# Kernel optimization log

Measured on AMD Instinct MI355X. Metric: run time of the kernel, lower is better.

## Reference

```python
import jax, jax.numpy as jnp
import numpy as np

H = 768       # hidden_size
HEADS = 8     # num_heads
T = 3         # num_timesteps
B = 128       # molecules in batch
N_ATOM = 48   # atoms per molecule
E_INTRA = 96  # intra-molecule directed edges per molecule
NPG = N_ATOM + 1          # nodes per graph (incl. virtual)
EPG = E_INTRA + N_ATOM    # edges per graph (incl. atom->virtual)
N = B * NPG
E = B * EPG


def setup_inputs() -> dict:
    key = jax.random.key(0)
    ks = jax.random.split(key, 10)
    atom_feat = jax.random.normal(ks[0], (B, N_ATOM, H), dtype=jnp.float32)
    mol_feat = jax.random.normal(ks[1], (B, H), dtype=jnp.float32)
    # node features with virtual node (=mol_feat) appended per graph, as in add_virtual_nodes_and_edges
    h_nodes = jnp.concatenate([atom_feat, mol_feat[:, None, :]], axis=1).reshape(N, H)
    off = jnp.arange(B, dtype=jnp.int32) * NPG
    intra_src = jax.random.randint(ks[2], (B, E_INTRA), 0, N_ATOM, dtype=jnp.int32) + off[:, None]
    intra_dst = jax.random.randint(ks[3], (B, E_INTRA), 0, N_ATOM, dtype=jnp.int32) + off[:, None]
    virt_src = jnp.arange(N_ATOM, dtype=jnp.int32)[None, :] + off[:, None]
    virt_dst = jnp.broadcast_to((off + N_ATOM)[:, None], (B, N_ATOM))
    src = jnp.concatenate([intra_src, virt_src], axis=1).reshape(E)
    dst = jnp.concatenate([intra_dst, virt_dst], axis=1).reshape(E)
    virtual_nids = off + N_ATOM  # last node of each graph (cumsum(batch_num_nodes)-1)
    attn_eids = ((jnp.arange(B, dtype=jnp.int32) * EPG)[:, None]
                 + E_INTRA + jnp.arange(N_ATOM, dtype=jnp.int32)[None, :]).reshape(-1)
    s = 0.02
    W_src = jax.random.normal(ks[4], (T, H, HEADS * H), dtype=jnp.float32) * s
    W_dst = jax.random.normal(ks[5], (T, H, HEADS * H), dtype=jnp.float32) * s
    attn_a = jax.random.normal(ks[6], (T, HEADS, H), dtype=jnp.float32) * s
    W_ih = jax.random.normal(ks[7], (T, 3 * H, H), dtype=jnp.float32) * s
    W_hh = jax.random.normal(ks[8], (T, 3 * H, H), dtype=jnp.float32) * s
    b_src = jnp.zeros((T, HEADS * H), jnp.float32)
    b_dst = jnp.zeros((T, HEADS * H), jnp.float32)
    b_ih = jnp.zeros((T, 3 * H), jnp.float32)
    b_hh = jnp.zeros((T, 3 * H), jnp.float32)
    return {"h_nodes": h_nodes, "mol_feat": mol_feat, "W_src": W_src, "b_src": b_src,
            "W_dst": W_dst, "b_dst": b_dst, "attn_a": attn_a, "W_ih": W_ih, "W_hh": W_hh,
            "b_ih": b_ih, "b_hh": b_hh, "src": src, "dst": dst,
            "virtual_nids": virtual_nids, "attn_eids": attn_eids}


def _gru_cell(x, hprev, W_ih_t, W_hh_t, b_ih_t, b_hh_t):
    # torch.nn.GRUCell: gates ordered r, z, n
    gi = x @ W_ih_t.T + b_ih_t
    gh = hprev @ W_hh_t.T + b_hh_t
    ir, iz, inn = jnp.split(gi, 3, axis=-1)
    hr, hz, hn = jnp.split(gh, 3, axis=-1)
    r = jax.nn.sigmoid(ir + hr)
    z = jax.nn.sigmoid(iz + hz)
    n = jnp.tanh(inn + r * hn)
    return (1.0 - z) * n + z * hprev


def _forward(h_nodes, mol_feat, W_src, b_src, W_dst, b_dst, attn_a,
             W_ih, W_hh, b_ih, b_hh, src, dst, virtual_nids, attn_eids):
    h = h_nodes
    mol_emb = mol_feat
    attns = []
    for t in range(T):
        # GATv2Conv (DGL, eval mode so feat_drop/attn_drop are identity)
        fs = (h @ W_src[t] + b_src[t]).reshape(N, HEADS, H)
        fd = (h @ W_dst[t] + b_dst[t]).reshape(N, HEADS, H)
        e = jax.nn.leaky_relu(fs[src] + fd[dst], negative_slope=0.2)  # [E, heads, H]
        logits = jnp.einsum('ehd,hd->eh', e, attn_a[t])               # [E, heads]
        # edge softmax over incoming edges per destination node
        m = jax.ops.segment_max(logits, dst, num_segments=N)
        ex = jnp.exp(logits - m[dst])
        ssum = jax.ops.segment_sum(ex, dst, num_segments=N)
        a = ex / ssum[dst]                                            # [E, heads]
        rst = jax.ops.segment_sum(a[:, :, None] * fs[src], dst, num_segments=N)  # [N, heads, H]
        h = rst.mean(axis=1)                                          # mean over heads
        out_virtual = h[virtual_nids]                                 # [B, H]
        mol_emb = jax.nn.relu(_gru_cell(out_virtual, mol_emb, W_ih[t], W_hh[t], b_ih[t], b_hh[t]))
        attns.append(a.mean(axis=1)[attn_eids])                       # attention on virtual edges
    return mol_emb, jnp.stack(attns)


def reference(h_nodes, mol_feat, W_src, b_src, W_dst, b_dst, attn_a,
              W_ih, W_hh, b_ih, b_hh, src, dst, virtual_nids, attn_eids):
    return _forward(h_nodes, mol_feat, W_src, b_src, W_dst, b_dst, attn_a,
                    W_ih, W_hh, b_ih, b_hh, src, dst, virtual_nids, attn_eids)
```

## Files before the change

kernel.cpp:

```cpp
#include <hip/hip_runtime.h>
#include <hip/hip_bf16.h>

typedef __hip_bfloat16 bf16;
typedef float f32x4 __attribute__((ext_vector_type(4)));
typedef __bf16 bf16x8 __attribute__((ext_vector_type(8)));
typedef short s16x8 __attribute__((ext_vector_type(8)));
typedef short s16x2 __attribute__((ext_vector_type(2)));

#define HDIM 768
#define NHEAD 8
#define BMOL 128
#define NPG 49
#define EPG 144
#define NNODE (BMOL * NPG)
#define NEDGE (BMOL * EPG)
#define NH 6144
#define G3 2304

__device__ __forceinline__ float b2f(short s) {
    unsigned int u = ((unsigned int)(unsigned short)s) << 16;
    return __builtin_bit_cast(float, u);
}

__device__ __forceinline__ void async16(const bf16* g, bf16* l) {
    __builtin_amdgcn_global_load_lds(
        (const __attribute__((address_space(1))) void*)g,
        (__attribute__((address_space(3))) void*)l, 16, 0, 0);
}

__global__ __launch_bounds__(256) void gemm_bt(
    const bf16* __restrict__ A, const bf16* __restrict__ Bt0,
    const bf16* __restrict__ Bt1, const float* __restrict__ bias0,
    const float* __restrict__ bias1, bf16* __restrict__ C0,
    bf16* __restrict__ C1, int M, int N, int K) {
    __shared__ __align__(16) bf16 lA[2 * 128 * 32];
    __shared__ __align__(16) bf16 lB[2 * 128 * 32];
    const int tid = threadIdx.x;
    const int lane = tid & 63;
    const int wave = tid >> 6;
    const int l16 = lane & 15;
    const int quad = lane >> 4;
    const int m0 = blockIdx.y * 128;
    const int n0 = blockIdx.x * 128;
    const bf16* Bt = blockIdx.z ? Bt1 : Bt0;
    const float* bias = blockIdx.z ? bias1 : bias0;
    bf16* C = blockIdx.z ? C1 : C0;

    const int r64 = tid >> 2;
    const int kc = (tid & 3) * 8;

    const bf16* gA = A + (size_t)(m0 + r64) * K + kc;
    const bf16* gB = Bt + (size_t)(n0 + r64) * K + kc;
    bf16* lAp = lA + tid * 8;
    bf16* lBp = lB + tid * 8;
    const size_t rstep = (size_t)64 * K;

    const int wm0 = (wave >> 1) * 64;
    const int wn0 = (wave & 1) * 64;

    f32x4 acc[4][4];
#pragma unroll
    for (int i = 0; i < 4; ++i)
#pragma unroll
        for (int j = 0; j < 4; ++j) acc[i][j] = (f32x4){0.f, 0.f, 0.f, 0.f};

    for (int k0 = 0; k0 < K; k0 += 64) {
        __syncthreads();
        async16(gA + k0, lAp);
        async16(gA + k0 + rstep, lAp + 2048);
        async16(gA + k0 + 32, lAp + 4096);
        async16(gA + k0 + 32 + rstep, lAp + 6144);
        async16(gB + k0, lBp);
        async16(gB + k0 + rstep, lBp + 2048);
        async16(gB + k0 + 32, lBp + 4096);
        async16(gB + k0 + 32 + rstep, lBp + 6144);
        __syncthreads();
#pragma unroll
        for (int ks = 0; ks < 2; ++ks) {
            bf16x8 af[4], bfr[4];
#pragma unroll
            for (int i = 0; i < 4; ++i)
                af[i] = *(const bf16x8*)(lA + ks * 4096 +
                                         (wm0 + i * 16 + l16) * 32 + quad * 8);
#pragma unroll
            for (int j = 0; j < 4; ++j)
                bfr[j] = *(const bf16x8*)(lB + ks * 4096 +
                                          (wn0 + j * 16 + l16) * 32 + quad * 8);
#pragma unroll
            for (int i = 0; i < 4; ++i)
#pragma unroll
                for (int j = 0; j < 4; ++j)
                    acc[i][j] = __builtin_amdgcn_mfma_f32_16x16x32_bf16(
                        af[i], bfr[j], acc[i][j], 0, 0, 0);
        }
    }

#pragma unroll
    for (int i = 0; i < 4; ++i) {
#pragma unroll
        for (int j = 0; j < 4; ++j) {
            int row = m0 + wm0 + i * 16 + quad * 4;
            int col = n0 + wn0 + j * 16 + l16;
            float bc = bias[col];
#pragma unroll
            for (int r = 0; r < 4; ++r)
                C[(size_t)(row + r) * N + col] =
                    __float2bfloat16(acc[i][j][r] + bc);
        }
    }
}

__global__ __launch_bounds__(256) void gemm_small(
    const bf16* __restrict__ hws, const int* __restrict__ vnids,
    const bf16* __restrict__ A1, const bf16* __restrict__ B0,
    const bf16* __restrict__ B1, const float* __restrict__ bias0,
    const float* __restrict__ bias1, float* __restrict__ C0,
    float* __restrict__ C1) {
    __shared__ __align__(16) bf16 lA[32 * 32];
    __shared__ __align__(16) bf16 lB[256 * 32];
    const int tid = threadIdx.x;
    const int lane = tid & 63;
    const int wave = tid >> 6;
    const int l16 = lane & 15;
    const int quad = lane >> 4;
    const int K = HDIM;
    const int y0 = blockIdx.y * 32;
    const int x0 = blockIdx.x * 256;
    const bf16* Bt = blockIdx.z ? B1 : B0;
    const float* bias = blockIdx.z ? bias1 : bias0;
    float* C = blockIdx.z ? C1 : C0;

    const int ry = y0 + (tid >> 2);
    const bf16* gA;
    if (blockIdx.z)
        gA = A1 + (size_t)ry * K + (tid & 3) * 8;
    else
        gA = hws + (size_t)vnids[ry & 127] * K + (tid & 3) * 8;
    const bf16* gB = Bt + (size_t)(x0 + (tid >> 2)) * K + (tid & 3) * 8;
    bf16* lAp = lA + tid * 8;
    bf16* lBp = lB + tid * 8;
    const size_t rstep = (size_t)64 * K;

    f32x4 acc[2][4];
#pragma unroll
    for (int i = 0; i < 2; ++i)
#pragma unroll
        for (int j = 0; j < 4; ++j) acc[i][j] = (f32x4){0.f, 0.f, 0.f, 0.f};

    for (int k0 = 0; k0 < K; k0 += 32) {
        __syncthreads();
        if (tid < 128) async16(gA + k0, lAp);
        async16(gB + k0, lBp);
        async16(gB + k0 + rstep, lBp + 2048);
        async16(gB + k0 + 2 * rstep, lBp + 4096);
        async16(gB + k0 + 3 * rstep, lBp + 6144);
        __syncthreads();
        bf16x8 af[2], bfr[4];
#pragma unroll
        for (int i = 0; i < 2; ++i)
            af[i] = *(const bf16x8*)(lA + (i * 16 + l16) * 32 + quad * 8);
#pragma unroll
        for (int j = 0; j < 4; ++j)
            bfr[j] = *(const bf16x8*)(lB + (wave * 64 + j * 16 + l16) * 32 +
                                      quad * 8);
#pragma unroll
        for (int i = 0; i < 2; ++i)
#pragma unroll
            for (int j = 0; j < 4; ++j)
                acc[i][j] = __builtin_amdgcn_mfma_f32_16x16x32_bf16(
                    af[i], bfr[j], acc[i][j], 0, 0, 0);
    }

#pragma unroll
    for (int i = 0; i < 2; ++i) {
#pragma unroll
        for (int j = 0; j < 4; ++j) {
            int row = y0 + i * 16 + quad * 4;
            int col = x0 + wave * 64 + j * 16 + l16;
            float bc = bias[col];
#pragma unroll
            for (int r = 0; r < 4; ++r)
                C[(size_t)(row + r) * G3 + col] = acc[i][j][r] + bc;
        }
    }
}

__global__ __launch_bounds__(256) void transpose_w(
    const float* __restrict__ W, bf16* __restrict__ Wt, int K, int Nn) {
    __shared__ bf16 tile[64][65];
    const int z = blockIdx.z;
    const float* Wp = W + (size_t)z * K * Nn;
    bf16* Wtp = Wt + (size_t)z * K * Nn;
    const int n0 = blockIdx.x * 64;
    const int k0 = blockIdx.y * 64;
    const int tx = threadIdx.x & 63;
    const int ty = threadIdx.x >> 6;
#pragma unroll
    for (int i = 0; i < 64; i += 4)
        tile[ty + i][tx] = __float2bfloat16(Wp[(size_t)(k0 + ty + i) * Nn + n0 + tx]);
    __syncthreads();
#pragma unroll
    for (int i = 0; i < 64; i += 4)
        Wtp[(size_t)(n0 + ty + i) * K + k0 + tx] = tile[tx][ty + i];
}

__global__ void cvt_kernel(const float* __restrict__ x, bf16* __restrict__ y,
                           int n) {
    int i = blockIdx.x * 256 + threadIdx.x;
    if (i < n) y[i] = __float2bfloat16(x[i]);
}

__global__ __launch_bounds__(256) void logits_kernel(
    const bf16* __restrict__ fs, const bf16* __restrict__ fd,
    const float* __restrict__ attn_a_t, const int* __restrict__ src,
    const int* __restrict__ dst, float* __restrict__ logits) {
    __shared__ __align__(16) float s_a[NH];
    const int tid = threadIdx.x;
    for (int p = tid; p < NH; p += 256) s_a[p] = attn_a_t[p];
    __syncthreads();

    const int wave = tid >> 6;
    const int lane = tid & 63;
    const int e = blockIdx.x * 4 + wave;
    const int gs = src[e], gd = dst[e];
    const bf16* ps = fs + (size_t)gs * NH;
    const bf16* pd = fd + (size_t)gd * NH;
    const int h = lane >> 3;
    const int s = lane & 7;
    const int base = h * HDIM + s * 8;

    float acc = 0.f;
#pragma unroll
    for (int j = 0; j < 12; ++j) {
        const int off = base + j * 64;
        s16x8 a8 = *(const s16x8*)(ps + off);
        s16x8 d8 = *(const s16x8*)(pd + off);
        f32x4 av0 = *(const f32x4*)(s_a + off);
        f32x4 av1 = *(const f32x4*)(s_a + off + 4);
#pragma unroll
        for (int u = 0; u < 4; ++u) {
            float x = b2f(a8[u]) + b2f(d8[u]);
            x = (x > 0.f) ? x : 0.2f * x;
            acc += x * av0[u];
        }
#pragma unroll
        for (int u = 0; u < 4; ++u) {
            float x = b2f(a8[4 + u]) + b2f(d8[4 + u]);
            x = (x > 0.f) ? x : 0.2f * x;
            acc += x * av1[u];
        }
    }
    acc += __shfl_xor(acc, 1);
    acc += __shfl_xor(acc, 2);
    acc += __shfl_xor(acc, 4);
    if (s == 0) logits[(size_t)e * NHEAD + h] = acc;
}

__global__ __launch_bounds__(256) void softmax_kernel(
    const float* __restrict__ logits, const int* __restrict__ dst,
    float* __restrict__ w, float* __restrict__ outv) {
    __shared__ float s_logit[EPG * NHEAD];
    __shared__ float s_w[EPG * NHEAD];
    __shared__ int s_ld[EPG];
    __shared__ float s_m[NPG * NHEAD], s_inv[NPG * NHEAD];
    const int tid = threadIdx.x;
    const int b = blockIdx.x;
    for (int p = tid; p < EPG * NHEAD; p += 256)
        s_logit[p] = logits[(size_t)b * EPG * NHEAD + p];
    if (tid < EPG) s_ld[tid] = dst[b * EPG + tid] - b * NPG;
    __syncthreads();

    for (int p = tid; p < NPG * NHEAD; p += 256) {
        int n = p >> 3, h = p & 7;
        float m = -3.0e38f;
        for (int le = 0; le < EPG; ++le)
            if (s_ld[le] == n) m = fmaxf(m, s_logit[le * NHEAD + h]);
        float ss = 0.f;
        for (int le = 0; le < EPG; ++le)
            if (s_ld[le] == n) ss += __expf(s_logit[le * NHEAD + h] - m);
        s_m[p] = m;
        s_inv[p] = (ss > 0.f) ? 1.f / ss : 0.f;
    }
    __syncthreads();

    for (int p = tid; p < EPG * NHEAD; p += 256) {
        int le = p >> 3, h = p & 7;
        int ld = s_ld[le];
        float a =
            0.125f * __expf(s_logit[p] - s_m[ld * NHEAD + h]) * s_inv[ld * NHEAD + h];
        s_w[p] = a;
        w[(size_t)b * EPG * NHEAD + p] = a;
    }
    __syncthreads();
    if (tid < 48) {
        float s = 0.f;
#pragma unroll
        for (int h = 0; h < NHEAD; ++h) s += s_w[(96 + tid) * NHEAD + h];
        outv[b * 48 + tid] = s;
    }
}

__global__ __launch_bounds__(256) void aggregate_kernel(
    const bf16* __restrict__ fs, const float* __restrict__ w,
    const int* __restrict__ src, const int* __restrict__ dst,
    bf16* __restrict__ hout) {
    __shared__ float acc[NPG * 128];
    __shared__ float s_w[EPG * NHEAD];
    __shared__ int s_gs[EPG], s_ld[EPG];
    const int tid = threadIdx.x;
    const int c = blockIdx.x;
    const int b = blockIdx.y;
    const int grp = tid >> 6;
    const int l = tid & 63;
    if (tid < EPG) {
        int e = b * EPG + tid;
        s_gs[tid] = src[e];
        s_ld[tid] = dst[e] - b * NPG;
    }
    for (int p = tid; p < EPG * NHEAD; p += 256)
        s_w[p] = w[(size_t)b * EPG * NHEAD + p];
    for (int p = tid; p < NPG * 128; p += 256) acc[p] = 0.f;
    __syncthreads();

    const int dim = c * 128 + l * 2;
    for (int le4 = 0; le4 < EPG; le4 += 4) {
        const int le = le4 + grp;
        const bf16* p = fs + (size_t)s_gs[le] * NH + dim;
        float sum0 = 0.f, sum1 = 0.f;
#pragma unroll
        for (int h = 0; h < NHEAD; ++h) {
            s16x2 v = *(const s16x2*)(p + h * HDIM);
            float wv = s_w[le * NHEAD + h];
            sum0 += wv * b2f(v[0]);
            sum1 += wv * b2f(v[1]);
        }
        float* ap = &acc[s_ld[le] * 128 + l * 2];
        atomicAdd(ap, sum0);
        atomicAdd(ap + 1, sum1);
    }
    __syncthreads();
    for (int p = tid; p < NPG * 128; p += 256) {
        int n = p >> 7, d = p & 127;
        hout[((size_t)b * NPG + n) * HDIM + c * 128 + d] =
            __float2bfloat16(acc[p]);
    }
}

__global__ void init_memb_kernel(const float* __restrict__ mf,
                                 float* __restrict__ m32,
                                 bf16* __restrict__ m16) {
    int idx = blockIdx.x * 256 + threadIdx.x;
    float f = mf[idx];
    m32[idx] = f;
    m16[idx] = __float2bfloat16(f);
}

__global__ void gru_gate_kernel(const float* __restrict__ gi,
                                const float* __restrict__ gh,
                                float* __restrict__ m32, bf16* __restrict__ m16,
                                float* __restrict__ outp, int last) {
    int idx = blockIdx.x * 256 + threadIdx.x;
    int b = idx / HDIM, d = idx - b * HDIM;
    const float* gib = gi + (size_t)b * G3;
    const float* ghb = gh + (size_t)b * G3;
    float ir = gib[d], iz = gib[HDIM + d], in_ = gib[2 * HDIM + d];
    float hr = ghb[d], hz = ghb[HDIM + d], hn = ghb[2 * HDIM + d];
    float r = 1.f / (1.f + __expf(-(ir + hr)));
    float z = 1.f / (1.f + __expf(-(iz + hz)));
    float n = tanhf(in_ + r * hn);
    float hprev = m32[idx];
    float hnew = (1.f - z) * n + z * hprev;
    hnew = fmaxf(hnew, 0.f);
    m32[idx] = hnew;
    m16[idx] = __float2bfloat16(hnew);
    if (last) outp[idx] = hnew;
}

extern "C" void kernel_launch(void* const* d_in, const int* in_sizes, int n_in,
                              void* d_out, int out_size, void* d_ws,
                              size_t ws_size, hipStream_t stream) {
    const float* h_nodes = (const float*)d_in[0];
    const float* mol_feat = (const float*)d_in[1];
    const float* W_src = (const float*)d_in[2];
    const float* b_src = (const float*)d_in[3];
    const float* W_dst = (const float*)d_in[4];
    const float* b_dst = (const float*)d_in[5];
    const float* attn_a = (const float*)d_in[6];
    const float* W_ih = (const float*)d_in[7];
    const float* W_hh = (const float*)d_in[8];
    const float* b_ih = (const float*)d_in[9];
    const float* b_hh = (const float*)d_in[10];
    const int* src = (const int*)d_in[11];
    const int* dst = (const int*)d_in[12];
    const int* vnids = (const int*)d_in[13];
    float* out = (float*)d_out;

    char* p = (char*)d_ws;
    auto alloc = [&](size_t bytes) {
        char* r = p;
        p += (bytes + 255) & ~(size_t)255;
        return r;
    };
    bf16* wsrcT = (bf16*)alloc((size_t)3 * NH * HDIM * 2);
    bf16* wdstT = (bf16*)alloc((size_t)3 * NH * HDIM * 2);
    bf16* wihB = (bf16*)alloc((size_t)3 * G3 * HDIM * 2);
    bf16* whhB = (bf16*)alloc((size_t)3 * G3 * HDIM * 2);
    bf16* fs = (bf16*)alloc((size_t)NNODE * NH * 2);
    bf16* fd = (bf16*)alloc((size_t)NNODE * NH * 2);
    bf16* h_ws = (bf16*)alloc((size_t)NNODE * HDIM * 2);
    float* lg = (float*)alloc((size_t)NEDGE * NHEAD * 4);
    float* w_e = (float*)alloc((size_t)NEDGE * NHEAD * 4);
    float* memb32 = (float*)alloc((size_t)BMOL * HDIM * 4);
    bf16* memb16 = (bf16*)alloc((size_t)BMOL * HDIM * 2);
    float* gi = (float*)alloc((size_t)BMOL * G3 * 4);
    float* gh = (float*)alloc((size_t)BMOL * G3 * 4);

    dim3 tgrid(NH / 64, HDIM / 64, 3);
    transpose_w<<<tgrid, 256, 0, stream>>>(W_src, wsrcT, HDIM, NH);
    transpose_w<<<tgrid, 256, 0, stream>>>(W_dst, wdstT, HDIM, NH);
    {
        int n = 3 * G3 * HDIM;
        cvt_kernel<<<(n + 255) / 256, 256, 0, stream>>>(W_ih, wihB, n);
        cvt_kernel<<<(n + 255) / 256, 256, 0, stream>>>(W_hh, whhB, n);
    }
    {
        int n = NNODE * HDIM;
        cvt_kernel<<<(n + 255) / 256, 256, 0, stream>>>(h_nodes, h_ws, n);
    }
    init_memb_kernel<<<BMOL * HDIM / 256, 256, 0, stream>>>(mol_feat, memb32,
                                                            memb16);

    for (int t = 0; t < 3; ++t) {
        gemm_bt<<<dim3(NH / 128, NNODE / 128, 2), 256, 0, stream>>>(
            h_ws, wsrcT + (size_t)t * NH * HDIM, wdstT + (size_t)t * NH * HDIM,
            b_src + (size_t)t * NH, b_dst + (size_t)t * NH, fs, fd, NNODE, NH,
            HDIM);
        logits_kernel<<<NEDGE / 4, 256, 0, stream>>>(
            fs, fd, attn_a + (size_t)t * NHEAD * HDIM, src, dst, lg);
        softmax_kernel<<<BMOL, 256, 0, stream>>>(
            lg, dst, w_e, out + BMOL * HDIM + t * BMOL * 48);
        aggregate_kernel<<<dim3(6, BMOL), 256, 0, stream>>>(fs, w_e, src, dst,
                                                            h_ws);
        gemm_small<<<dim3(G3 / 256, 4, 2), 256, 0, stream>>>(
            h_ws, vnids, memb16, wihB + (size_t)t * G3 * HDIM,
            whhB + (size_t)t * G3 * HDIM, b_ih + (size_t)t * G3,
            b_hh + (size_t)t * G3, gi, gh);
        gru_gate_kernel<<<BMOL * HDIM / 256, 256, 0, stream>>>(
            gi, gh, memb32, memb16, out, t == 2);
    }
}
```

Before: 1.206 ms.

## Replace node-projection GEMM with 256x256 double-buffered pipelined 8-wave kernel

Replaces the 128x128 single-buffered bf16 GEMM, which syncs twice per k-step, with a 256x256 tile, 512-thread kernel. It double-buffers LDS through async global-to-LDS loads interleaved with MFMA phases, uses XOR-swizzled LDS layouts to avoid bank conflicts, and remaps block IDs for L2 locality. The epilogue stages output through LDS so stores are coalesced 16-byte writes, and rows past the edge are clamped. It uses 128 KB of LDS per block and a hand-tuned vmcnt schedule, which is fragile and may limit occupancy.

```diff
diff --git a/kernel.cpp b/kernel.cpp
--- a/kernel.cpp
+++ b/kernel.cpp
@@ -28,86 +28,178 @@
         (__attribute__((address_space(3))) void*)l, 16, 0, 0);
 }
 
-__global__ __launch_bounds__(256) void gemm_bt(
+#define VMCNT(n) asm volatile("s_waitcnt vmcnt(" #n ")" ::: "memory")
+#define SBAR()                                 \
+    do {                                       \
+        asm volatile("" ::: "memory");         \
+        __builtin_amdgcn_s_barrier();          \
+        asm volatile("" ::: "memory");         \
+    } while (0)
+
+__global__ __launch_bounds__(512, 2) void gemm_bt8(
     const bf16* __restrict__ A, const bf16* __restrict__ Bt0,
     const bf16* __restrict__ Bt1, const float* __restrict__ bias0,
     const float* __restrict__ bias1, bf16* __restrict__ C0,
-    bf16* __restrict__ C1, int M, int N, int K) {
-    __shared__ __align__(16) bf16 lA[2 * 128 * 32];
-    __shared__ __align__(16) bf16 lB[2 * 128 * 32];
+    bf16* __restrict__ C1) {
+    __shared__ __align__(16) char smem[131072];
+    bf16* lA = (bf16*)smem;
+    bf16* lB = (bf16*)(smem + 65536);
+
     const int tid = threadIdx.x;
     const int lane = tid & 63;
     const int wave = tid >> 6;
     const int l16 = lane & 15;
     const int quad = lane >> 4;
-    const int m0 = blockIdx.y * 128;
-    const int n0 = blockIdx.x * 128;
+    const int wm = wave >> 2;
+    const int wn = wave & 3;
+    const int K = HDIM;
+
+    int id = blockIdx.y * 24 + blockIdx.x;
+    int swz = (id & 7) * 75 + (id >> 3);
+    const int m0 = (swz / 24) * 256;
+    const int n0 = (swz % 24) * 256;
+
     const bf16* Bt = blockIdx.z ? Bt1 : Bt0;
     const float* bias = blockIdx.z ? bias1 : bias0;
     bf16* C = blockIdx.z ? C1 : C0;
 
-    const int r64 = tid >> 2;
-    const int kc = (tid & 3) * 8;
-
-    const bf16* gA = A + (size_t)(m0 + r64) * K + kc;
-    const bf16* gB = Bt + (size_t)(n0 + r64) * K + kc;
-    bf16* lAp = lA + tid * 8;
-    bf16* lBp = lB + tid * 8;
-    const size_t rstep = (size_t)64 * K;
-
-    const int wm0 = (wave >> 1) * 64;
-    const int wn0 = (wave & 1) * 64;
-
-    f32x4 acc[4][4];
-#pragma unroll
-    for (int i = 0; i < 4; ++i)
+    const int srow = tid >> 3;
+    const int ecol = ((tid & 7) * 8) ^ ((srow & 4) ? 16 : 0);
+    const bf16* gAr[4];
+#pragma unroll
+    for (int hc = 0; hc < 4; ++hc) {
+        int r = m0 + srow + hc * 64;
+        if (r > NNODE - 1) r = NNODE - 1;
+        gAr[hc] = A + (size_t)r * K + ecol;
+    }
+    const bf16* gB = Bt + (size_t)(n0 + srow) * K + ecol;
+    const size_t hstep = (size_t)128 * K;
+    const size_t cstep = (size_t)64 * K;
+    bf16* dA = lA + tid * 8;
+    bf16* dB = lB + tid * 8;
+
+#define STAGE_A(buf, h, kt)                                     \
+    do {                                                        \
+        bf16* _d = dA + (buf)*16384 + (h)*8192;                 \
+        async16(gAr[(h)*2] + (size_t)(kt) * 64, _d);            \
+        async16(gAr[(h)*2 + 1] + (size_t)(kt) * 64, _d + 4096); \
+    } while (0)
+#define STAGE_B(buf, h, kt)                                     \
+    do {                                                        \
+        const bf16* _s = gB + (h)*hstep + (size_t)(kt) * 64;    \
+        bf16* _d = dB + (buf)*16384 + (h)*8192;                 \
+        async16(_s, _d);                                        \
+        async16(_s + cstep, _d + 4096);                         \
+    } while (0)
+
+    const int aq = (quad * 16) ^ ((l16 & 4) << 3);
+    const char* laB = (const char*)lA + wm * 16384 + l16 * 128 + aq;
+    const char* lbB =
+        (const char*)lB + (wn >> 1) * 16384 + (wn & 1) * 8192 + l16 * 128 + aq;
+
+#define LDA8(buf, f, ks) \
+    (*(const bf16x8*)(laB + (buf)*32768 + (f)*2048 + (ks)*64))
+#define LDB8(buf, j, ks) \
+    (*(const bf16x8*)(lbB + (buf)*32768 + (j)*2048 + (ks)*64))
+
+    f32x4 acc[8][4];
+#pragma unroll
+    for (int i = 0; i < 8; ++i)
 #pragma unroll
         for (int j = 0; j < 4; ++j) acc[i][j] = (f32x4){0.f, 0.f, 0.f, 0.f};
-
-    for (int k0 = 0; k0 < K; k0 += 64) {
-        __syncthreads();
-        async16(gA + k0, lAp);
-        async16(gA + k0 + rstep, lAp + 2048);
-        async16(gA + k0 + 32, lAp + 4096);
-        async16(gA + k0 + 32 + rstep, lAp + 6144);
-        async16(gB + k0, lBp);
-        async16(gB + k0 + rstep, lBp + 2048);
-        async16(gB + k0 + 32, lBp + 4096);
-        async16(gB + k0 + 32 + rstep, lBp + 6144);
-        __syncthreads();
-#pragma unroll
-        for (int ks = 0; ks < 2; ++ks) {
-            bf16x8 af[4], bfr[4];
-#pragma unroll
-            for (int i = 0; i < 4; ++i)
-                af[i] = *(const bf16x8*)(lA + ks * 4096 +
-                                         (wm0 + i * 16 + l16) * 32 + quad * 8);
-#pragma unroll
-            for (int j = 0; j < 4; ++j)
-                bfr[j] = *(const bf16x8*)(lB + ks * 4096 +
-                                          (wn0 + j * 16 + l16) * 32 + quad * 8);
-#pragma unroll
-            for (int i = 0; i < 4; ++i)
-#pragma unroll
-                for (int j = 0; j < 4; ++j)
-                    acc[i][j] = __builtin_amdgcn_mfma_f32_16x16x32_bf16(
-                        af[i], bfr[j], acc[i][j], 0, 0, 0);
+    bf16x8 bfr[4][2];
+
+#define MF(i, j, ks, areg)                                             \
+    acc[i][j] = __builtin_amdgcn_mfma_f32_16x16x32_bf16(areg, bfr[j][ks], \
+                                                        acc[i][j], 0, 0, 0)
+
+#define PHASE(buf, q, LB, STG, WAIT)                                   \
+    do {                                                               \
+        bf16x8 a00 = LDA8(buf, (q)*2, 0);                              \
+        bf16x8 a01 = LDA8(buf, (q)*2, 1);                              \
+        bf16x8 a10 = LDA8(buf, (q)*2 + 1, 0);                          \
+        bf16x8 a11 = LDA8(buf, (q)*2 + 1, 1);                          \
+        if (LB) {                                                      \
+            bfr[0][0] = LDB8(buf, 0, 0); bfr[0][1] = LDB8(buf, 0, 1);  \
+            bfr[1][0] = LDB8(buf, 1, 0); bfr[1][1] = LDB8(buf, 1, 1);  \
+            bfr[2][0] = LDB8(buf, 2, 0); bfr[2][1] = LDB8(buf, 2, 1);  \
+            bfr[3][0] = LDB8(buf, 3, 0); bfr[3][1] = LDB8(buf, 3, 1);  \
+        }                                                              \
+        STG;                                                           \
+        SBAR();                                                        \
+        __builtin_amdgcn_s_setprio(1);                                 \
+        MF((q)*2, 0, 0, a00); MF((q)*2, 1, 0, a00);                    \
+        MF((q)*2, 2, 0, a00); MF((q)*2, 3, 0, a00);                    \
+        MF((q)*2 + 1, 0, 0, a10); MF((q)*2 + 1, 1, 0, a10);            \
+        MF((q)*2 + 1, 2, 0, a10); MF((q)*2 + 1, 3, 0, a10);            \
+        MF((q)*2, 0, 1, a01); MF((q)*2, 1, 1, a01);                    \
+        MF((q)*2, 2, 1, a01); MF((q)*2, 3, 1, a01);                    \
+        MF((q)*2 + 1, 0, 1, a11); MF((q)*2 + 1, 1, 1, a11);            \
+        MF((q)*2 + 1, 2, 1, a11); MF((q)*2 + 1, 3, 1, a11);            \
+        __builtin_amdgcn_s_setprio(0);                                 \
+        WAIT;                                                          \
+        SBAR();                                                        \
+    } while (0)
+
+    STAGE_A(0, 0, 0); STAGE_A(0, 1, 0);
+    STAGE_B(0, 0, 0); STAGE_B(0, 1, 0);
+    STAGE_B(1, 0, 1); STAGE_B(1, 1, 1);
+    VMCNT(4);
+    SBAR();
+
+    int t0 = 0;
+    for (int it = 0; it < 5; ++it, t0 += 2) {
+        PHASE(0, 0, 1, STAGE_A(1, 0, t0 + 1), );
+        PHASE(0, 1, 0, STAGE_A(1, 1, t0 + 1), );
+        PHASE(0, 2, 0, STAGE_B(0, 0, t0 + 2), );
+        PHASE(0, 3, 0, STAGE_B(0, 1, t0 + 2), VMCNT(4));
+        PHASE(1, 0, 1, STAGE_A(0, 0, t0 + 2), );
+        PHASE(1, 1, 0, STAGE_A(0, 1, t0 + 2), );
+        PHASE(1, 2, 0, STAGE_B(1, 0, t0 + 3), );
+        PHASE(1, 3, 0, STAGE_B(1, 1, t0 + 3), VMCNT(4));
+    }
+    PHASE(0, 0, 1, STAGE_A(1, 0, 11), );
+    PHASE(0, 1, 0, STAGE_A(1, 1, 11), );
+    PHASE(0, 2, 0, , );
+    PHASE(0, 3, 0, , VMCNT(0));
+    PHASE(1, 0, 1, , );
+    PHASE(1, 1, 0, , );
+    PHASE(1, 2, 0, , );
+    PHASE(1, 3, 0, , );
+
+    __syncthreads();
+#pragma unroll
+    for (int i = 0; i < 8; ++i) {
+        const int rloc = wm * 128 + i * 16 + quad * 4;
+#pragma unroll
+        for (int j = 0; j < 4; ++j) {
+            const int cloc = wn * 64 + j * 16 + l16;
+            const float bc = bias[n0 + cloc];
+#pragma unroll
+            for (int r = 0; r < 4; ++r) {
+                const int rr = rloc + r;
+                int off = (rr * 512 + cloc * 2) ^ ((rr & 4) ? 32 : 0);
+                *(bf16*)(smem + off) = __float2bfloat16(acc[i][j][r] + bc);
+            }
         }
     }
-
-#pragma unroll
-    for (int i = 0; i < 4; ++i) {
-#pragma unroll
-        for (int j = 0; j < 4; ++j) {
-            int row = m0 + wm0 + i * 16 + quad * 4;
-            int col = n0 + wn0 + j * 16 + l16;
-            float bc = bias[col];
-#pragma unroll
-            for (int r = 0; r < 4; ++r)
-                C[(size_t)(row + r) * N + col] =
-                    __float2bfloat16(acc[i][j][r] + bc);
+    __syncthreads();
+#pragma unroll
+    for (int k = 0; k < 16; ++k) {
+        const int off = (k * 512 + tid) * 16;
+        const int row = off >> 9;
+        const int bcol = (off & 511) ^ ((row & 4) ? 32 : 0);
+        if (m0 + row < NNODE) {
+            bf16x8 v = *(const bf16x8*)(smem + off);
+            *(bf16x8*)(C + (size_t)(m0 + row) * NH + n0 + (bcol >> 1)) = v;
         }
     }
+#undef PHASE
+#undef MF
+#undef LDA8
+#undef LDB8
+#undef STAGE_A
+#undef STAGE_B
 }
 
 __global__ __launch_bounds__(256) void gemm_small(
@@ -431,10 +523,9 @@
                                                             memb16);
 
     for (int t = 0; t < 3; ++t) {
-        gemm_bt<<<dim3(NH / 128, NNODE / 128, 2), 256, 0, stream>>>(
+        gemm_bt8<<<dim3(24, 25, 2), 512, 0, stream>>>(
             h_ws, wsrcT + (size_t)t * NH * HDIM, wdstT + (size_t)t * NH * HDIM,
-            b_src + (size_t)t * NH, b_dst + (size_t)t * NH, fs, fd, NNODE, NH,
-            HDIM);
+            b_src + (size_t)t * NH, b_dst + (size_t)t * NH, fs, fd);
         logits_kernel<<<NEDGE / 4, 256, 0, stream>>>(
             fs, fd, attn_a + (size_t)t * NHEAD * HDIM, src, dst, lg);
         softmax_kernel<<<BMOL, 256, 0, stream>>>(
```

Result: no change. 1.214 ms (+0.6%).
